# Performance work log

Measured on AMD Instinct MI355X. Metric: run time of the kernel, lower is better.

## Reference

```python
import jax, jax.numpy as jnp
import numpy as np

EMBED_DIM = 1024
NUM_HEADS = 16
HEAD_DIM = EMBED_DIM // NUM_HEADS
B, S = 2, 2048


def setup_inputs() -> dict:
    key = jax.random.key(0)
    ks = jax.random.split(key, 5)
    scale = 1.0 / np.sqrt(EMBED_DIM)
    return {
        "inputs": jax.random.normal(ks[0], (B, S, EMBED_DIM), dtype=jnp.float32),
        "Wq": jax.random.normal(ks[1], (EMBED_DIM, EMBED_DIM), dtype=jnp.float32) * scale,
        "bq": jnp.zeros((EMBED_DIM,), dtype=jnp.float32),
        "Wk": jax.random.normal(ks[2], (EMBED_DIM, EMBED_DIM), dtype=jnp.float32) * scale,
        "bk": jnp.zeros((EMBED_DIM,), dtype=jnp.float32),
        "Wv": jax.random.normal(ks[3], (EMBED_DIM, EMBED_DIM), dtype=jnp.float32) * scale,
        "bv": jnp.zeros((EMBED_DIM,), dtype=jnp.float32),
        "Wo": jax.random.normal(ks[4], (EMBED_DIM, EMBED_DIM), dtype=jnp.float32) * scale,
        "bo": jnp.zeros((EMBED_DIM,), dtype=jnp.float32),
    }


def _split_heads(x):
    # [B, S, E] -> [B, H, S, Dh]
    b, s, _ = x.shape
    return x.reshape(b, s, NUM_HEADS, HEAD_DIM).transpose(0, 2, 1, 3)


def reference(inputs, Wq, bq, Wk, bk, Wv, bv, Wo, bo):
    q = _split_heads(inputs @ Wq + bq)  # [B, H, S, Dh]
    k = _split_heads(inputs @ Wk + bk)
    v = _split_heads(inputs @ Wv + bv)
    scale = 1.0 / jnp.sqrt(jnp.asarray(HEAD_DIM, dtype=q.dtype))
    scores = jnp.einsum("bhqd,bhkd->bhqk", q, k) * scale  # [B, H, S, S]
    weights = jax.nn.softmax(scores, axis=-1)
    attn = jnp.einsum("bhqk,bhkd->bhqd", weights, v)  # [B, H, S, Dh]
    concat = attn.transpose(0, 2, 1, 3).reshape(inputs.shape[0], -1, EMBED_DIM)
    return concat @ Wo + bo
```

## Files before the change

### kernel.cpp

```cpp
#include <hip/hip_runtime.h>


#define QSCALE 0.18033688011112042f

using bf16x8 = __attribute__((ext_vector_type(8))) short;
using f32x16 = __attribute__((ext_vector_type(16))) float;
using u16x8  = __attribute__((ext_vector_type(8))) unsigned short;

__device__ __forceinline__ unsigned short f2bf(float f) {
  unsigned int u = __float_as_uint(f);
  u += 0x7fffu + ((u >> 16) & 1u);
  return (unsigned short)(u >> 16);
}

__device__ __forceinline__ void gload_lds16(const unsigned short* g, unsigned short* l) {
  __builtin_amdgcn_global_load_lds(
      (const __attribute__((address_space(1))) unsigned int*)g,
      (__attribute__((address_space(3))) unsigned int*)l, 16, 0, 0);
}

__global__ void conv_x_kernel(const float* __restrict__ x, unsigned short* __restrict__ y) {
  int i = blockIdx.x * blockDim.x + threadIdx.x;
  const float4* xf = (const float4*)x;
  float4 a = xf[i * 2], b = xf[i * 2 + 1];
  u16x8 o;
  o[0] = f2bf(a.x); o[1] = f2bf(a.y); o[2] = f2bf(a.z); o[3] = f2bf(a.w);
  o[4] = f2bf(b.x); o[5] = f2bf(b.y); o[6] = f2bf(b.z); o[7] = f2bf(b.w);
  *((u16x8*)y + i) = o;
}

__global__ void conv_wT_kernel(const float* __restrict__ W0, const float* __restrict__ W1,
                               const float* __restrict__ W2, const float* __restrict__ W3,
                               unsigned short* __restrict__ out) {
  __shared__ float t[32][33];
  int z = blockIdx.z;
  const float* W = (z == 0) ? W0 : (z == 1) ? W1 : (z == 2) ? W2 : W3;
  unsigned short* o = out + (size_t)z * 1024 * 1024;
  int kt = blockIdx.y * 32, nt = blockIdx.x * 32;
  int tx = threadIdx.x, ty = threadIdx.y;
#pragma unroll
  for (int i = 0; i < 4; ++i)
    t[ty + i * 8][tx] = W[(size_t)(kt + ty + i * 8) * 1024 + nt + tx];
  __syncthreads();
#pragma unroll
  for (int i = 0; i < 4; ++i)
    o[(size_t)(nt + ty + i * 8) * 1024 + kt + tx] = f2bf(t[tx][ty + i * 8]);
}

__global__ __launch_bounds__(256) void gemm_bt_kernel(
    const unsigned short* __restrict__ A, const unsigned short* __restrict__ Bt,
    int mode, const float* __restrict__ bias0, const float* __restrict__ bias1,
    const float* __restrict__ bias2, unsigned short* __restrict__ Qh,
    unsigned short* __restrict__ Kh, unsigned short* __restrict__ Vt,
    float* __restrict__ Out) {
  const int K = 1024;
  __shared__ unsigned short SMEM[16384];

  int n0 = blockIdx.x * 128, m0 = blockIdx.y * 128;
  int tid = threadIdx.x;
  int w = tid >> 6, lane = tid & 63, l31 = lane & 31, half = lane >> 5;
  int wm = w >> 1, wn = w & 1;

  f32x16 acc[2][2];
#pragma unroll
  for (int i = 0; i < 2; ++i)
#pragma unroll
    for (int j = 0; j < 2; ++j)
#pragma unroll
      for (int r = 0; r < 16; ++r) acc[i][j][r] = 0.f;

  int srow = lane >> 2;
  int gchunk = (lane & 3) ^ (srow & 3);
  const unsigned short* Ag = A + (size_t)(m0 + 32 * w + srow) * K + gchunk * 8;
  const unsigned short* Bg = Bt + (size_t)(n0 + 32 * w + srow) * K + gchunk * 8;
  unsigned short* Asw = &SMEM[w * 1024];
  unsigned short* Bsw = &SMEM[8192 + w * 1024];

#pragma unroll
  for (int j = 0; j < 2; ++j) {
    gload_lds16(Ag + (size_t)(16 * j) * K, Asw + j * 512);
    gload_lds16(Bg + (size_t)(16 * j) * K, Bsw + j * 512);
  }

  for (int it = 0; it < 32; ++it) {
    int cur = (it & 1) * 4096;
    __syncthreads();
    if (it + 1 < 32) {
      int nxt = ((it + 1) & 1) * 4096;
      int kk = (it + 1) * 32;
#pragma unroll
      for (int j = 0; j < 2; ++j) {
        gload_lds16(Ag + kk + (size_t)(16 * j) * K, Asw + nxt + j * 512);
        gload_lds16(Bg + kk + (size_t)(16 * j) * K, Bsw + nxt + j * 512);
      }
    }
    const unsigned short* Asl = &SMEM[cur];
    const unsigned short* Bsl = &SMEM[8192 + cur];
#pragma unroll
    for (int kc = 0; kc < 2; ++kc) {
      int ph = ((kc * 2 + half) ^ (l31 & 3)) * 8;
      bf16x8 af[2], bfr[2];
#pragma unroll
      for (int mt = 0; mt < 2; ++mt)
        af[mt] = *(bf16x8*)&Asl[(wm * 64 + mt * 32 + l31) * 32 + ph];
#pragma unroll
      for (int nt = 0; nt < 2; ++nt)
        bfr[nt] = *(bf16x8*)&Bsl[(wn * 64 + nt * 32 + l31) * 32 + ph];
#pragma unroll
      for (int mt = 0; mt < 2; ++mt)
#pragma unroll
        for (int nt = 0; nt < 2; ++nt)
          acc[mt][nt] = __builtin_amdgcn_mfma_f32_32x32x16_bf16(af[mt], bfr[nt], acc[mt][nt], 0, 0, 0);
    }
  }

  if (mode == 1) {
#pragma unroll
    for (int mt = 0; mt < 2; ++mt)
#pragma unroll
      for (int nt = 0; nt < 2; ++nt)
#pragma unroll
        for (int r = 0; r < 16; ++r) {
          int row = (r & 3) + 8 * (r >> 2) + 4 * half;
          int gm = m0 + wm * 64 + mt * 32 + row;
          int gn = n0 + wn * 64 + nt * 32 + l31;
          Out[(size_t)gm * 1024 + gn] = acc[mt][nt][r] + bias0[gn];
        }
    return;
  }

  int btype = blockIdx.x >> 3;
  if (btype < 2) {
    const float* bp = btype ? bias1 : bias0;
    unsigned short* dst = btype ? Kh : Qh;
    float sc = btype ? 1.0f : QSCALE;
#pragma unroll
    for (int mt = 0; mt < 2; ++mt)
#pragma unroll
      for (int nt = 0; nt < 2; ++nt)
#pragma unroll
        for (int r = 0; r < 16; ++r) {
          int row = (r & 3) + 8 * (r >> 2) + 4 * half;
          int gm = m0 + wm * 64 + mt * 32 + row;
          int gn = n0 + wn * 64 + nt * 32 + l31;
          int e = gn & 1023;
          float v = (acc[mt][nt][r] + bp[e]) * sc;
          int hh = e >> 6, d = e & 63;
          int bb = gm >> 11, s = gm & 2047;
          dst[(((size_t)(bb * 16 + hh)) * 2048 + s) * 64 + d] = f2bf(v);
        }
  } else {
    __syncthreads();
    unsigned short* T = SMEM;
#pragma unroll
    for (int mt = 0; mt < 2; ++mt)
#pragma unroll
      for (int nt = 0; nt < 2; ++nt)
#pragma unroll
        for (int r = 0; r < 16; ++r) {
          int row = (r & 3) + 8 * (r >> 2) + 4 * half;
          int sl = wm * 64 + mt * 32 + row;
          int dl = wn * 64 + nt * 32 + l31;
          int e = (n0 - 2048) + dl;
          float v = acc[mt][nt][r] + bias2[e];
          T[dl * 128 + (sl ^ ((dl & 15) << 3))] = f2bf(v);
        }
    __syncthreads();
    int bb = m0 >> 11, s0 = m0 & 2047;
    int h0 = (n0 - 2048) >> 6;
    int rr0 = tid >> 2, csub = tid & 3;
#pragma unroll
    for (int pass = 0; pass < 2; ++pass) {
      int rr = rr0 + 64 * pass;
      int hh = h0 + (rr >> 6), d = rr & 63;
      unsigned short* vrow = Vt + (((size_t)(bb * 16 + hh)) * 64 + d) * 2048 + s0;
#pragma unroll
      for (int c = 0; c < 4; ++c) {
        int cc = c * 4 + csub;
        uint4 val = *(uint4*)&T[rr * 128 + ((cc ^ (rr & 15)) * 8)];
        *(uint4*)&vrow[cc * 8] = val;
      }
    }
  }
}

__global__ __launch_bounds__(512, 4) void attn_kernel(
    const unsigned short* __restrict__ Qh, const unsigned short* __restrict__ Kh,
    const unsigned short* __restrict__ Vt, unsigned short* __restrict__ Ctx) {
  __shared__ __align__(16) unsigned short SM[32768];

  int qt = blockIdx.x, h = blockIdx.y, b = blockIdx.z;
  int tid = threadIdx.x;
  int w = tid >> 6, lane = tid & 63, l31 = lane & 31, half = lane >> 5;
  int l7 = l31 & 7;
  int mw = w & 3, kw = w >> 2;

  size_t bh = (size_t)(b * 16 + h);
  const unsigned short* Qb  = Qh + (bh * 2048 + qt * 128) * 64;
  const unsigned short* Kbh = Kh + bh * 131072;
  const unsigned short* Vbh = Vt + bh * 131072;

  bf16x8 qf[4];
#pragma unroll
  for (int kc = 0; kc < 4; ++kc)
    qf[kc] = *(const bf16x8*)&Qb[(size_t)(mw * 32 + l31) * 64 + kc * 16 + half * 8];

  int r8 = lane >> 3, cl = lane & 7, gc = cl ^ r8;
  const unsigned short* gb[4];
  int lofs[4], gstep[4];
#pragma unroll
  for (int j = 0; j < 4; ++j) {
    int g = w * 4 + j, t = g >> 3, s = g & 7;
    if (t < 2) { gb[j] = Kbh + (size_t)(t * 1024 + s * 8 + r8) * 64 + gc * 8; gstep[j] = 4096; }
    else       { gb[j] = Vbh + (size_t)(s * 8 + r8) * 2048 + (t - 2) * 1024 + gc * 8; gstep[j] = 64; }
    lofs[j] = t * 4096 + s * 512;
  }
#pragma unroll
  for (int j = 0; j < 4; ++j) { gload_lds16(gb[j], SM + lofs[j]); gb[j] += gstep[j]; }

  f32x16 o0, o1;
#pragma unroll
  for (int r = 0; r < 16; ++r) { o0[r] = 0.f; o1[r] = 0.f; }
  float l_acc = 0.f;

  for (int i = 0; i < 16; ++i) {
    __syncthreads();
    if (i < 15) {
      unsigned short* nb = SM + (((i + 1) & 1) << 14);
#pragma unroll
      for (int j = 0; j < 4; ++j) { gload_lds16(gb[j], nb + lofs[j]); gb[j] += gstep[j]; }
    }
    const unsigned short* cur = SM + ((i & 1) << 14);
    const unsigned short* Ksw = cur + kw * 4096;
    const unsigned short* Vsw = cur + 8192 + kw * 4096;

    f32x16 st0, st1;
#pragma unroll
    for (int r = 0; r < 16; ++r) { st0[r] = 0.f; st1[r] = 0.f; }
#pragma unroll
    for (int kc = 0; kc < 4; ++kc) {
      int ph = ((kc * 2 + half) ^ l7) * 8;
      bf16x8 kb0 = *(bf16x8*)&Ksw[l31 * 64 + ph];
      bf16x8 kb1 = *(bf16x8*)&Ksw[(32 + l31) * 64 + ph];
      st0 = __builtin_amdgcn_mfma_f32_32x32x16_bf16(kb0, qf[kc], st0, 0, 0, 0);
      st1 = __builtin_amdgcn_mfma_f32_32x32x16_bf16(kb1, qf[kc], st1, 0, 0, 0);
    }

    float pt0[16], pt1[16];
    float ladd = 0.f;
#pragma unroll
    for (int r = 0; r < 16; ++r) {
      pt0[r] = exp2f(st0[r]);
      pt1[r] = exp2f(st1[r]);
      ladd += pt0[r] + pt1[r];
    }
    l_acc += ladd;

    unsigned int own[16];
#pragma unroll
    for (int m = 0; m < 4; ++m)
#pragma unroll
      for (int p = 0; p < 2; ++p) {
        int r = 4 * m + 2 * p;
        own[2 * m + p]     = __builtin_amdgcn_perm(__float_as_uint(pt0[r + 1]), __float_as_uint(pt0[r]), 0x07060302u);
        own[2 * m + 8 + p] = __builtin_amdgcn_perm(__float_as_uint(pt1[r + 1]), __float_as_uint(pt1[r]), 0x07060302u);
      }
    unsigned int rcv[16];
#pragma unroll
    for (int j = 0; j < 16; ++j) rcv[j] = (unsigned int)__shfl_xor((int)own[j], 32);

#pragma unroll
    for (int kc = 0; kc < 4; ++kc) {
      union { unsigned int u[4]; bf16x8 v; } U;
      U.u[0] = half ? rcv[4 * kc + 2] : own[4 * kc];
      U.u[1] = half ? rcv[4 * kc + 3] : own[4 * kc + 1];
      U.u[2] = half ? own[4 * kc + 2] : rcv[4 * kc];
      U.u[3] = half ? own[4 * kc + 3] : rcv[4 * kc + 1];
      int ph = ((kc * 2 + half) ^ l7) * 8;
      bf16x8 vb0 = *(bf16x8*)&Vsw[l31 * 64 + ph];
      bf16x8 vb1 = *(bf16x8*)&Vsw[(32 + l31) * 64 + ph];
      o0 = __builtin_amdgcn_mfma_f32_32x32x16_bf16(U.v, vb0, o0, 0, 0, 0);
      o1 = __builtin_amdgcn_mfma_f32_32x32x16_bf16(U.v, vb1, o1, 0, 0, 0);
    }
  }

  float lw = l_acc + __shfl_xor(l_acc, 32);
  __syncthreads();
  float* mrgO = (float*)SM;
  float* mrgL = (float*)SM + 8192;
  if (kw == 1) {
    float* dst = mrgO + mw * 2048 + lane * 32;
#pragma unroll
    for (int c = 0; c < 8; ++c) {
      float4 t;
      if (c < 4) t = make_float4(o0[4 * c], o0[4 * c + 1], o0[4 * c + 2], o0[4 * c + 3]);
      else       t = make_float4(o1[4 * (c - 4)], o1[4 * (c - 4) + 1], o1[4 * (c - 4) + 2], o1[4 * (c - 4) + 3]);
      *(float4*)&dst[(c ^ l7) * 4] = t;
    }
    if (half == 0) mrgL[mw * 32 + l31] = lw;
  }
  __syncthreads();
  if (kw == 0) {
    const float* src = mrgO + mw * 2048 + lane * 32;
#pragma unroll
    for (int c = 0; c < 8; ++c) {
      float4 t = *(const float4*)&src[(c ^ l7) * 4];
      if (c < 4) { o0[4 * c] += t.x; o0[4 * c + 1] += t.y; o0[4 * c + 2] += t.z; o0[4 * c + 3] += t.w; }
      else       { o1[4 * (c - 4)] += t.x; o1[4 * (c - 4) + 1] += t.y; o1[4 * (c - 4) + 2] += t.z; o1[4 * (c - 4) + 3] += t.w; }
    }
    lw += mrgL[mw * 32 + l31];
    float inv = 1.0026f / lw;
#pragma unroll
    for (int r = 0; r < 16; ++r) {
      int rmap = (r & 3) + 8 * (r >> 2) + 4 * half;
      float invr = __shfl(inv, rmap);
      size_t row = (size_t)(b * 2048 + qt * 128 + mw * 32 + rmap);
      Ctx[row * 1024 + h * 64 + l31]      = f2bf(o0[r] * invr);
      Ctx[row * 1024 + h * 64 + 32 + l31] = f2bf(o1[r] * invr);
    }
  }
}

extern "C" void kernel_launch(void* const* d_in, const int* in_sizes, int n_in,
                              void* d_out, int out_size, void* d_ws, size_t ws_size,
                              hipStream_t stream) {
  const float* X  = (const float*)d_in[0];
  const float* Wq = (const float*)d_in[1];
  const float* bq = (const float*)d_in[2];
  const float* Wk = (const float*)d_in[3];
  const float* bk = (const float*)d_in[4];
  const float* Wv = (const float*)d_in[5];
  const float* bv = (const float*)d_in[6];
  const float* Wo = (const float*)d_in[7];
  const float* bo = (const float*)d_in[8];

  if (ws_size < (size_t)48 * 1024 * 1024) return;

  char* ws = (char*)d_ws;
  unsigned short* Xbf = (unsigned short*)(ws);
  unsigned short* Wt  = (unsigned short*)(ws + ((size_t)8 << 20));
  unsigned short* Qh  = (unsigned short*)(ws + ((size_t)16 << 20));
  unsigned short* Kh  = (unsigned short*)(ws + ((size_t)24 << 20));
  unsigned short* Vt  = (unsigned short*)(ws + ((size_t)32 << 20));
  unsigned short* Ctx = (unsigned short*)(ws + ((size_t)40 << 20));
  unsigned short* WtO = Wt + (size_t)3 * 1024 * 1024;

  conv_x_kernel<<<2048, 256, 0, stream>>>(X, Xbf);
  conv_wT_kernel<<<dim3(32, 32, 4), dim3(32, 8), 0, stream>>>(Wq, Wk, Wv, Wo, Wt);
  gemm_bt_kernel<<<dim3(24, 32), 256, 0, stream>>>(Xbf, Wt, 0, bq, bk, bv, Qh, Kh, Vt, nullptr);
  attn_kernel<<<dim3(16, 16, 2), 512, 0, stream>>>(Qh, Kh, Vt, Ctx);
  gemm_bt_kernel<<<dim3(8, 32), 256, 0, stream>>>(Ctx, WtO, 1, bo, bo, bo, nullptr, nullptr, nullptr, (float*)d_out);
}
```

Measured before the change: 213.7 us.

## Fuse conversion kernels and remove cross-lane shuffle from attention P·V

Merges the activation bf16 conversion and the weight transpose-conversion into a single launch, removing one kernel launch. In the attention inner loop it drops the 16 per-iteration xor-32 shuffles that redistributed P between lane halves. Instead each lane keeps its own P fragment and loads V from LDS as two 8-byte pieces whose offsets depend on the lane half, so the MFMA reduction ordering matches. It also seeds the first QK MFMA from a zero vector and accumulates the row sums in a packed float2. The risk is that the changed V load pattern brings LDS bank conflicts or more LDS instructions.

```diff
diff --git a/kernel.cpp b/kernel.cpp
--- a/kernel.cpp
+++ b/kernel.cpp
@@ -5,6 +5,7 @@
 
 using bf16x8 = __attribute__((ext_vector_type(8))) short;
 using f32x16 = __attribute__((ext_vector_type(16))) float;
+using f32x2  = __attribute__((ext_vector_type(2))) float;
 using u16x8  = __attribute__((ext_vector_type(8))) unsigned short;
 
 __device__ __forceinline__ unsigned short f2bf(float f) {
@@ -19,25 +20,28 @@
       (__attribute__((address_space(3))) unsigned int*)l, 16, 0, 0);
 }
 
-__global__ void conv_x_kernel(const float* __restrict__ x, unsigned short* __restrict__ y) {
-  int i = blockIdx.x * blockDim.x + threadIdx.x;
-  const float4* xf = (const float4*)x;
-  float4 a = xf[i * 2], b = xf[i * 2 + 1];
-  u16x8 o;
-  o[0] = f2bf(a.x); o[1] = f2bf(a.y); o[2] = f2bf(a.z); o[3] = f2bf(a.w);
-  o[4] = f2bf(b.x); o[5] = f2bf(b.y); o[6] = f2bf(b.z); o[7] = f2bf(b.w);
-  *((u16x8*)y + i) = o;
-}
-
-__global__ void conv_wT_kernel(const float* __restrict__ W0, const float* __restrict__ W1,
-                               const float* __restrict__ W2, const float* __restrict__ W3,
-                               unsigned short* __restrict__ out) {
+__global__ void conv_fused_kernel(const float* __restrict__ X, unsigned short* __restrict__ Xbf,
+                                  const float* __restrict__ W0, const float* __restrict__ W1,
+                                  const float* __restrict__ W2, const float* __restrict__ W3,
+                                  unsigned short* __restrict__ Wt) {
   __shared__ float t[32][33];
-  int z = blockIdx.z;
+  int blk = blockIdx.x, tid = threadIdx.x;
+  if (blk < 2048) {
+    int i = blk * 256 + tid;
+    const float4* xf = (const float4*)X;
+    float4 a = xf[i * 2], b = xf[i * 2 + 1];
+    u16x8 o;
+    o[0] = f2bf(a.x); o[1] = f2bf(a.y); o[2] = f2bf(a.z); o[3] = f2bf(a.w);
+    o[4] = f2bf(b.x); o[5] = f2bf(b.y); o[6] = f2bf(b.z); o[7] = f2bf(b.w);
+    *((u16x8*)Xbf + i) = o;
+    return;
+  }
+  int zb = blk - 2048;
+  int z = zb >> 10, rem = zb & 1023;
+  int nt = (rem & 31) * 32, kt = (rem >> 5) * 32;
   const float* W = (z == 0) ? W0 : (z == 1) ? W1 : (z == 2) ? W2 : W3;
-  unsigned short* o = out + (size_t)z * 1024 * 1024;
-  int kt = blockIdx.y * 32, nt = blockIdx.x * 32;
-  int tx = threadIdx.x, ty = threadIdx.y;
+  unsigned short* o = Wt + (size_t)z * 1024 * 1024;
+  int tx = tid & 31, ty = tid >> 5;
 #pragma unroll
   for (int i = 0; i < 4; ++i)
     t[ty + i * 8][tx] = W[(size_t)(kt + ty + i * 8) * 1024 + nt + tx];
@@ -218,10 +222,10 @@
 #pragma unroll
   for (int j = 0; j < 4; ++j) { gload_lds16(gb[j], SM + lofs[j]); gb[j] += gstep[j]; }
 
-  f32x16 o0, o1;
-#pragma unroll
-  for (int r = 0; r < 16; ++r) { o0[r] = 0.f; o1[r] = 0.f; }
-  float l_acc = 0.f;
+  f32x16 o0, o1, z16;
+#pragma unroll
+  for (int r = 0; r < 16; ++r) { o0[r] = 0.f; o1[r] = 0.f; z16[r] = 0.f; }
+  f32x2 lp; lp[0] = 0.f; lp[1] = 0.f;
 
   for (int i = 0; i < 16; ++i) {
     __syncthreads();
@@ -236,53 +240,52 @@
 
     f32x16 st0, st1;
 #pragma unroll
-    for (int r = 0; r < 16; ++r) { st0[r] = 0.f; st1[r] = 0.f; }
-#pragma unroll
     for (int kc = 0; kc < 4; ++kc) {
       int ph = ((kc * 2 + half) ^ l7) * 8;
       bf16x8 kb0 = *(bf16x8*)&Ksw[l31 * 64 + ph];
       bf16x8 kb1 = *(bf16x8*)&Ksw[(32 + l31) * 64 + ph];
-      st0 = __builtin_amdgcn_mfma_f32_32x32x16_bf16(kb0, qf[kc], st0, 0, 0, 0);
-      st1 = __builtin_amdgcn_mfma_f32_32x32x16_bf16(kb1, qf[kc], st1, 0, 0, 0);
-    }
-
-    float pt0[16], pt1[16];
-    float ladd = 0.f;
-#pragma unroll
-    for (int r = 0; r < 16; ++r) {
-      pt0[r] = exp2f(st0[r]);
-      pt1[r] = exp2f(st1[r]);
-      ladd += pt0[r] + pt1[r];
-    }
-    l_acc += ladd;
+      if (kc == 0) {
+        st0 = __builtin_amdgcn_mfma_f32_32x32x16_bf16(kb0, qf[0], z16, 0, 0, 0);
+        st1 = __builtin_amdgcn_mfma_f32_32x32x16_bf16(kb1, qf[0], z16, 0, 0, 0);
+      } else {
+        st0 = __builtin_amdgcn_mfma_f32_32x32x16_bf16(kb0, qf[kc], st0, 0, 0, 0);
+        st1 = __builtin_amdgcn_mfma_f32_32x32x16_bf16(kb1, qf[kc], st1, 0, 0, 0);
+      }
+    }
+
+    f32x2 p0v[8], p1v[8];
+#pragma unroll
+    for (int j = 0; j < 8; ++j) {
+      p0v[j][0] = exp2f(st0[2 * j]); p0v[j][1] = exp2f(st0[2 * j + 1]);
+      p1v[j][0] = exp2f(st1[2 * j]); p1v[j][1] = exp2f(st1[2 * j + 1]);
+      lp += p0v[j]; lp += p1v[j];
+    }
 
     unsigned int own[16];
 #pragma unroll
-    for (int m = 0; m < 4; ++m)
-#pragma unroll
-      for (int p = 0; p < 2; ++p) {
-        int r = 4 * m + 2 * p;
-        own[2 * m + p]     = __builtin_amdgcn_perm(__float_as_uint(pt0[r + 1]), __float_as_uint(pt0[r]), 0x07060302u);
-        own[2 * m + 8 + p] = __builtin_amdgcn_perm(__float_as_uint(pt1[r + 1]), __float_as_uint(pt1[r]), 0x07060302u);
-      }
-    unsigned int rcv[16];
-#pragma unroll
-    for (int j = 0; j < 16; ++j) rcv[j] = (unsigned int)__shfl_xor((int)own[j], 32);
+    for (int j = 0; j < 8; ++j) {
+      own[j]     = __builtin_amdgcn_perm(__float_as_uint(p0v[j][1]), __float_as_uint(p0v[j][0]), 0x07060302u);
+      own[8 + j] = __builtin_amdgcn_perm(__float_as_uint(p1v[j][1]), __float_as_uint(p1v[j][0]), 0x07060302u);
+    }
 
 #pragma unroll
     for (int kc = 0; kc < 4; ++kc) {
       union { unsigned int u[4]; bf16x8 v; } U;
-      U.u[0] = half ? rcv[4 * kc + 2] : own[4 * kc];
-      U.u[1] = half ? rcv[4 * kc + 3] : own[4 * kc + 1];
-      U.u[2] = half ? own[4 * kc + 2] : rcv[4 * kc];
-      U.u[3] = half ? own[4 * kc + 3] : rcv[4 * kc + 1];
-      int ph = ((kc * 2 + half) ^ l7) * 8;
-      bf16x8 vb0 = *(bf16x8*)&Vsw[l31 * 64 + ph];
-      bf16x8 vb1 = *(bf16x8*)&Vsw[(32 + l31) * 64 + ph];
-      o0 = __builtin_amdgcn_mfma_f32_32x32x16_bf16(U.v, vb0, o0, 0, 0, 0);
-      o1 = __builtin_amdgcn_mfma_f32_32x32x16_bf16(U.v, vb1, o1, 0, 0, 0);
-    }
-  }
+      U.u[0] = own[4 * kc];     U.u[1] = own[4 * kc + 1];
+      U.u[2] = own[4 * kc + 2]; U.u[3] = own[4 * kc + 3];
+      int phA = ((2 * kc) ^ l7) * 8 + 4 * half;
+      int phB = ((2 * kc + 1) ^ l7) * 8 + 4 * half;
+      union { unsigned long long q[2]; bf16x8 v; } V0, V1;
+      V0.q[0] = *(const unsigned long long*)&Vsw[l31 * 64 + phA];
+      V0.q[1] = *(const unsigned long long*)&Vsw[l31 * 64 + phB];
+      V1.q[0] = *(const unsigned long long*)&Vsw[(32 + l31) * 64 + phA];
+      V1.q[1] = *(const unsigned long long*)&Vsw[(32 + l31) * 64 + phB];
+      o0 = __builtin_amdgcn_mfma_f32_32x32x16_bf16(U.v, V0.v, o0, 0, 0, 0);
+      o1 = __builtin_amdgcn_mfma_f32_32x32x16_bf16(U.v, V1.v, o1, 0, 0, 0);
+    }
+  }
+
+  float l_acc = lp[0] + lp[1];
 
   float lw = l_acc + __shfl_xor(l_acc, 32);
   __syncthreads();
@@ -345,8 +348,7 @@
   unsigned short* Ctx = (unsigned short*)(ws + ((size_t)40 << 20));
   unsigned short* WtO = Wt + (size_t)3 * 1024 * 1024;
 
-  conv_x_kernel<<<2048, 256, 0, stream>>>(X, Xbf);
-  conv_wT_kernel<<<dim3(32, 32, 4), dim3(32, 8), 0, stream>>>(Wq, Wk, Wv, Wo, Wt);
+  conv_fused_kernel<<<6144, 256, 0, stream>>>(X, Xbf, Wq, Wk, Wv, Wo, Wt);
   gemm_bt_kernel<<<dim3(24, 32), 256, 0, stream>>>(Xbf, Wt, 0, bq, bk, bv, Qh, Kh, Vt, nullptr);
   attn_kernel<<<dim3(16, 16, 2), 512, 0, stream>>>(Qh, Kh, Vt, Ctx);
   gemm_bt_kernel<<<dim3(8, 32), 256, 0, stream>>>(Ctx, WtO, 1, bo, bo, bo, nullptr, nullptr, nullptr, (float*)d_out);
```

Measured after the change: 215.8 us. Within noise of the previous version (+1.0%).
